# Optimization experiments

Hardware: AMD Instinct MI355X
Metric: run time of the kernel (lower is better)

Reference implementation:

```python
import jax, jax.numpy as jnp
import numpy as np

NODE_NUM = 6
C_IN = 1024
B = 16384
N_OPS = 9
TAU = 10.0
EPS = 1e-5
ACTS = (jax.nn.relu, jax.nn.sigmoid, jnp.tanh)


def setup_inputs() -> dict:
    key = jax.random.key(0)
    k = jax.random.split(key, 12)
    n_edges = NODE_NUM * (NODE_NUM + 1) // 2  # 21
    nB = n_edges - NODE_NUM  # 15 edges with cin=cout=C_IN//2

    def w(kk, shape, fan_in):
        return jax.random.normal(kk, shape, jnp.float32) / np.float32(np.sqrt(fan_in))

    return {
        "x": jax.random.normal(k[0], (B, C_IN), jnp.float32),
        "arch_params": 0.001 * jax.random.normal(k[1], (n_edges, N_OPS), jnp.float32),
        "gumbel": jax.random.gumbel(k[2], (n_edges, N_OPS), jnp.float32),
        "dense_w_A": w(k[3], (NODE_NUM, 3, C_IN // 2, C_IN), C_IN),
        "dense_b_A": 0.01 * jax.random.normal(k[4], (NODE_NUM, 3, C_IN // 2), jnp.float32),
        "group_w_A": w(k[5], (NODE_NUM, 3, 4, C_IN // 8, C_IN // 4), C_IN // 4),
        "group_b_A": 0.01 * jax.random.normal(k[6], (NODE_NUM, 3, C_IN // 2), jnp.float32),
        "pool_w_A": w(k[7], (NODE_NUM, 2, C_IN // 2, C_IN), C_IN),
        "dense_w_B": w(k[8], (nB, 3, C_IN // 2, C_IN // 2), C_IN // 2),
        "dense_b_B": 0.01 * jax.random.normal(k[9], (nB, 3, C_IN // 2), jnp.float32),
        "group_w_B": w(k[10], (nB, 3, 4, C_IN // 8, C_IN // 8), C_IN // 8),
        "group_b_B": 0.01 * jax.random.normal(k[11], (nB, 3, C_IN // 2), jnp.float32),
    }


def _batchnorm(h):
    # training-mode BatchNorm2d on [B, C, 1, 1] == normalize over batch, affine-free
    m = jnp.mean(h, axis=0, keepdims=True)
    v = jnp.var(h, axis=0, keepdims=True)
    return (h - m) * jax.lax.rsqrt(v + EPS)


def _apply_edge(h, op_idx, wscale, dw, db, gw, gb, pw):
    # h: [B, cin]; dw: [3, cout, cin]; gw: [3, 4, cout//4, cin//4]; pw: [2, cout, cin] or None
    cout = dw.shape[1]

    def pool(p):
        def f(hh):
            # ReLU-Conv1x1-BN preprocess when cin != cout, else identity
            y = _batchnorm(jax.nn.relu(hh) @ pw[p].T) if pw is not None else hh
            if p == 0:  # avg_pool_3x3 on 1x1 spatial, pad=1, count_include_pad
                y = y / 9.0
            # p == 1: max_pool_3x3 on 1x1 spatial is identity
            return _batchnorm(y)  # MixedOp-appended BatchNorm2d(affine=False)
        return f

    def dense(a):
        return lambda hh: ACTS[a](hh @ dw[a].T + db[a])

    def gdense(a):
        def f(hh):
            hg = hh.reshape(hh.shape[0], 4, -1)  # [B, 4, cin//4]
            y = jnp.einsum('bgi,goi->bgo', hg, gw[a]).reshape(hh.shape[0], -1) + gb[a]
            return ACTS[a](y)
        return f

    zero = lambda hh: jnp.zeros((hh.shape[0], cout), hh.dtype)
    branches = [pool(0), pool(1), dense(0), dense(1), dense(2),
                gdense(0), gdense(1), gdense(2), zero]
    return jax.lax.switch(op_idx, branches, h) * wscale


def reference(x, arch_params, gumbel, dense_w_A, dense_b_A, group_w_A, group_b_A,
              pool_w_A, dense_w_B, dense_b_B, group_w_B, group_b_B):
    # GDAS gumbel-softmax hard routing (straight-through)
    logits = (jax.nn.log_softmax(arch_params, axis=1) + gumbel) / TAU
    prob = jax.nn.softmax(logits, axis=1)
    index = jnp.argmax(prob, axis=1)                      # [n_edges]
    one_h = jax.nn.one_hot(index, N_OPS, dtype=prob.dtype)
    hardwts = one_h - jax.lax.stop_gradient(prob) + prob  # [n_edges, N_OPS]

    # arch rows are indexed by sorted edge-key order, matching torch edge2index
    keys = sorted('{}->{}'.format(j, i + 1) for i in range(NODE_NUM) for j in range(i + 1))
    e2i = {kk: n for n, kk in enumerate(keys)}

    states = [x]
    a_ct = 0
    b_ct = 0
    for i in range(1, NODE_NUM + 1):
        acc = None
        for j in range(i):
            e = e2i['{}->{}'.format(j, i)]
            w_e = hardwts[e, index[e]]
            if j == 0:
                out = _apply_edge(states[0], index[e], w_e, dense_w_A[a_ct], dense_b_A[a_ct],
                                  group_w_A[a_ct], group_b_A[a_ct], pool_w_A[a_ct])
                a_ct += 1
            else:
                out = _apply_edge(states[j], index[e], w_e, dense_w_B[b_ct], dense_b_B[b_ct],
                                  group_w_B[b_ct], group_b_B[b_ct], None)
                b_ct += 1
            acc = out if acc is None else acc + out
        states.append(acc)
    return states[-1]  # [B, C_IN//2]; final_linear is never applied in forward()
```

## Files before the change

### kernel.cpp

```cpp
#include <hip/hip_runtime.h>

#define BATCH 16384
#define CH 512
#define EPSBN 1e-5f

typedef __attribute__((ext_vector_type(8))) short short8;
typedef __attribute__((ext_vector_type(4))) float f32x4;
typedef __attribute__((ext_vector_type(4))) unsigned short ushort4v;

#define GLOAD16(gp, lp) __builtin_amdgcn_global_load_lds( \
    (const __attribute__((address_space(1))) void*)(gp),  \
    (__attribute__((address_space(3))) void*)(lp), 16, 0, 0)

__constant__ int d_etab[6][6] = {
  {0,0,0,0,0,0},
  {1,6,0,0,0,0},
  {2,7,11,0,0,0},
  {3,8,12,15,0,0},
  {4,9,13,16,18,0},
  {5,10,14,17,19,20}};
__constant__ int d_bct[21] = {0,0,0,0,0,0, 0,1,3,6,10, 2,4,7,11, 5,8,12, 9,13, 14};

static __device__ __forceinline__ long woff(int e){
  return (e < 6) ? (long)e*524288 : 3145728L + (long)d_bct[e]*262144;
}

static __device__ __forceinline__ unsigned short f2b(float f){
  union { float f; unsigned u; } v; v.f = f;
  unsigned r = v.u + 0x7fffu + ((v.u >> 16) & 1u);
  return (unsigned short)(r >> 16);
}
static __device__ __forceinline__ float b2f(unsigned short u){
  union { unsigned u; float f; } v; v.u = ((unsigned)u) << 16; return v.f;
}
static __device__ __forceinline__ float actf(int act, float v){
  if (act == 0) return fmaxf(v, 0.f);
  if (act == 1) return 1.f/(1.f + __expf(-v));
  float e = __expf(2.f*v);
  return 1.f - 2.f/(e + 1.f);
}

__global__ void k_sentinel(float* out){ out[0] = 1.0e6f; }

__global__ void k_index(const float* __restrict__ ap, const float* __restrict__ gum,
                        int* __restrict__ idx, float* __restrict__ wsc){
  int e = threadIdx.x;
  if (e >= 21) return;
  const float* a = ap + e*9;
  const float* g = gum + e*9;
  float m = a[0];
  for (int o=1;o<9;o++) m = fmaxf(m, a[o]);
  float s = 0.f;
  for (int o=0;o<9;o++) s += expf(a[o]-m);
  float lse = m + logf(s);
  float lg[9]; float lm = -1e30f;
  for (int o=0;o<9;o++){ lg[o] = (a[o]-lse+g[o]) / 10.0f; lm = fmaxf(lm, lg[o]); }
  float ss = 0.f;
  for (int o=0;o<9;o++) ss += expf(lg[o]-lm);
  int bi = 0; float bp = -1.f;
  for (int o=0;o<9;o++){
    float p = expf(lg[o]-lm)/ss;
    if (p > bp){ bp = p; bi = o; }
  }
  idx[e] = bi;
  wsc[e] = (1.0f - bp) + bp;
}

__global__ void k_f2b4(const float* __restrict__ in, unsigned short* __restrict__ outp, long n4){
  long stride = (long)gridDim.x*blockDim.x;
  for (long i = (long)blockIdx.x*blockDim.x + threadIdx.x; i < n4; i += stride){
    const float4 v = ((const float4*)in)[i];
    ushort4v o;
    o[0] = f2b(v.x); o[1] = f2b(v.y); o[2] = f2b(v.z); o[3] = f2b(v.w);
    ((ushort4v*)outp)[i] = o;
  }
}

__global__ void k_wconv_all(const int* __restrict__ idxp,
                            const float* __restrict__ dwA, const float* __restrict__ pwA,
                            const float* __restrict__ gwA, const float* __restrict__ dwB,
                            const float* __restrict__ gwB,
                            unsigned short* __restrict__ Wball){
  int e = blockIdx.x >> 7;
  int blk = blockIdx.x & 127;
  int id = idxp[e];
  const float* src; long n;
  if (e < 6){
    int a = e;
    if (id >= 2 && id <= 4){ n = 524288; src = dwA + ((long)a*3 + (id-2))*n; }
    else if (id < 2)       { n = 524288; src = pwA + ((long)a*2 + id)*n; }
    else if (id <= 7)      { n = 131072; src = gwA + ((long)a*3 + (id-5))*131072; }
    else return;
  } else {
    int b = d_bct[e];
    if (id >= 2 && id <= 4)     { n = 262144; src = dwB + ((long)b*3 + (id-2))*n; }
    else if (id >= 5 && id <= 7){ n = 65536;  src = gwB + ((long)b*3 + (id-5))*65536; }
    else return;
  }
  unsigned short* dst = Wball + woff(e);
  long n4 = n >> 2;
  long stride = 128*256;
  for (long i = (long)blk*256 + threadIdx.x; i < n4; i += stride){
    const float4 v = ((const float4*)src)[i];
    ushort4v o;
    o[0] = f2b(v.x); o[1] = f2b(v.y); o[2] = f2b(v.z); o[3] = f2b(v.w);
    ((ushort4v*)dst)[i] = o;
  }
}

__global__ __launch_bounds__(512, 4) void k_gemmA_all(
    const unsigned short* __restrict__ xb, const unsigned short* __restrict__ Wball,
    unsigned short* __restrict__ s0, unsigned short* __restrict__ s1,
    unsigned short* __restrict__ s2, unsigned short* __restrict__ s3,
    unsigned short* __restrict__ s4, unsigned short* __restrict__ pre6,
    const float* __restrict__ dbA, const float* __restrict__ gbA,
    const int* __restrict__ idxp, const float* __restrict__ wscp)
{
  int e = blockIdx.x >> 9;
  int id = idxp[e];
  if (id == 8) return;
  unsigned short* target;
  switch(e){ case 0: target=s0; break; case 1: target=s1; break; case 2: target=s2; break;
             case 3: target=s3; break; case 4: target=s4; break; default: target=pre6; }
  bool pool = (id < 2);
  bool grp = (id >= 5);
  int K = grp ? 256 : 1024;
  int act = pool ? 0 : (grp ? id-5 : id-2);
  float we = wscp[e];

  int inner = blockIdx.x & 511;
  int lg = (inner & 7) * 64 + (inner >> 3);
  int rowTile = lg >> 2, colTile = lg & 3;
  int row0 = rowTile * 128, col0 = colTile * 128;

  int t = threadIdx.x;
  int lane = t & 63, wave = t >> 6;
  int wm = wave >> 2, wn = wave & 3;
  int l16 = lane & 15, lq = lane >> 4;

  __shared__ unsigned short LDS[24576];

  int ra = t >> 2;
  int ca = (((t & 3) ^ ((ra >> 1) & 3)) << 3);
  int aoff[4], boff[2];
  #pragma unroll
  for (int m=0;m<4;m++){ int R = wm*64 + m*16 + l16; aoff[m] = R*32 + ((lq ^ ((R>>1)&3))<<3); }
  #pragma unroll
  for (int n=0;n<2;n++){ int C = wn*32 + n*16 + l16; boff[n] = C*32 + ((lq ^ ((C>>1)&3))<<3); }

  const unsigned short* Abase = xb + (grp ? (long)colTile*K : 0);
  const unsigned short* Wbase = Wball + (long)e*524288 + (long)col0*K;
  const unsigned short* gA = Abase + (long)(row0 + ra)*1024 + ca;
  const unsigned short* gB = Wbase + (long)ra*K + ca;
  const float* bias = (grp ? gbA : dbA) + ((long)e*3 + act)*CH;

  f32x4 acc[4][2];
  #pragma unroll
  for (int m=0;m<4;m++){ acc[m][0]=(f32x4){0,0,0,0}; acc[m][1]=(f32x4){0,0,0,0}; }

  auto STAGE = [&](int tile, int bsel){
    long kk = (long)tile*32;
    GLOAD16(gA + kk, &LDS[bsel*4096 + t*8]);
    GLOAD16(gB + kk, &LDS[12288 + bsel*4096 + t*8]);
  };

  int nk = K >> 5;
  STAGE(0, 0);
  STAGE(1, 1);
  int cb = 0;
  for (int kt = 0; kt < nk; ++kt){
    if (kt+1 < nk) { asm volatile("s_waitcnt vmcnt(2)" ::: "memory"); }
    else           { asm volatile("s_waitcnt vmcnt(0)" ::: "memory"); }
    __builtin_amdgcn_s_barrier();
    if (kt+2 < nk) STAGE(kt+2, (cb >= 1) ? cb-1 : cb+2);
    const unsigned short* pA = &LDS[cb*4096];
    const unsigned short* pB = &LDS[12288 + cb*4096];
    short8 a[4], b[2];
    #pragma unroll
    for (int m=0;m<4;m++){
      a[m] = *(const short8*)(pA + aoff[m]);
      if (pool){
        #pragma unroll
        for (int q=0;q<8;q++) a[m][q] = (a[m][q] < (short)0) ? (short)0 : a[m][q];
      }
    }
    #pragma unroll
    for (int n=0;n<2;n++) b[n] = *(const short8*)(pB + boff[n]);
    #pragma unroll
    for (int m=0;m<4;m++)
      #pragma unroll
      for (int n=0;n<2;n++)
        acc[m][n] = __builtin_amdgcn_mfma_f32_16x16x32_bf16(a[m], b[n], acc[m][n], 0,0,0);
    cb = (cb+1 == 3) ? 0 : cb+1;
  }

  #pragma unroll
  for (int n=0;n<2;n++){
    int cn = col0 + wn*32 + n*16 + l16;
    float bv = pool ? 0.f : bias[cn];
    #pragma unroll
    for (int m=0;m<4;m++)
      #pragma unroll
      for (int r=0;r<4;r++){
        int row = row0 + wm*64 + m*16 + lq*4 + r;
        long off = (long)row*CH + cn;
        if (pool) target[off] = f2b(acc[m][n][r]);
        else      target[off] = f2b(we * actf(act, acc[m][n][r] + bv));
      }
  }
}

__global__ __launch_bounds__(512) void k_statsA(
    const unsigned short* __restrict__ s0, const unsigned short* __restrict__ s1,
    const unsigned short* __restrict__ s2, const unsigned short* __restrict__ s3,
    const unsigned short* __restrict__ s4, const unsigned short* __restrict__ pre6,
    float* __restrict__ part, const int* __restrict__ idxp)
{
  int e = blockIdx.x >> 7;
  if (idxp[e] >= 2) return;
  const unsigned short* S;
  switch(e){ case 0: S=s0; break; case 1: S=s1; break; case 2: S=s2; break;
             case 3: S=s3; break; case 4: S=s4; break; default: S=pre6; }
  int blk = blockIdx.x & 127;
  int c = threadIdx.x;
  const unsigned short* p = S + (long)blk*128*CH + c;
  float s = 0.f, q = 0.f;
  for (int r = 0; r < 128; r++){ float v = b2f(p[(long)r*CH]); s += v; q += v*v; }
  long o = (((long)e*128 + blk)*CH + c)*2;
  part[o] = s; part[o+1] = q;
}

__global__ __launch_bounds__(512) void k_stats2A(
    const float* __restrict__ part, float* __restrict__ alphaAll,
    float* __restrict__ mvalAll, const int* __restrict__ idxp)
{
  int c = threadIdx.x;
  for (int e = 0; e < 6; ++e){
    int id = idxp[e];
    if (id >= 2) continue;
    float s = 0.f, q = 0.f;
    for (int b = 0; b < 128; b++){
      long o = (((long)e*128 + b)*CH + c)*2;
      s += part[o]; q += part[o+1];
    }
    float m = s * (1.f/16384.f);
    float v = q * (1.f/16384.f) - m*m;
    v = fmaxf(v, 0.f);
    float s1 = rsqrtf(v + EPSBN);
    float vz = v / (v + EPSBN);
    float al = (id==0) ? (s1 * (1.f/9.f) * rsqrtf(vz*(1.f/81.f) + EPSBN))
                       : (s1 * rsqrtf(vz + EPSBN));
    alphaAll[(long)e*CH + c] = al;
    mvalAll[(long)e*CH + c] = m;
  }
}

__global__ __launch_bounds__(512) void k_statsB_node(
    int node,
    const unsigned short* __restrict__ sb0, const unsigned short* __restrict__ sb1,
    const unsigned short* __restrict__ sb2, const unsigned short* __restrict__ sb3,
    const unsigned short* __restrict__ sb4,
    float* __restrict__ part, const int* __restrict__ idxp)
{
  int c = threadIdx.x;
  for (int jj = 1; jj < node; ++jj){
    int e = d_etab[node-1][jj];
    if (idxp[e] >= 2) continue;
    const unsigned short* S;
    switch(jj){ case 1: S=sb0; break; case 2: S=sb1; break;
                case 3: S=sb2; break; case 4: S=sb3; break; default: S=sb4; }
    const unsigned short* p = S + (long)blockIdx.x*128*CH + c;
    float s = 0.f, q = 0.f;
    for (int r = 0; r < 128; r++){ float v = b2f(p[(long)r*CH]); s += v; q += v*v; }
    long o = (((long)jj*128 + blockIdx.x)*CH + c)*2;
    part[o] = s; part[o+1] = q;
  }
}

__global__ __launch_bounds__(512) void k_stats2B_node(
    int node, const float* __restrict__ part,
    float* __restrict__ alphaAll, float* __restrict__ mvalAll,
    const int* __restrict__ idxp)
{
  int c = threadIdx.x;
  for (int jj = 1; jj < node; ++jj){
    int e = d_etab[node-1][jj];
    int id = idxp[e];
    if (id >= 2) continue;
    float s = 0.f, q = 0.f;
    for (int b = 0; b < 128; b++){
      long o = (((long)jj*128 + b)*CH + c)*2;
      s += part[o]; q += part[o+1];
    }
    float m = s * (1.f/16384.f);
    float v = q * (1.f/16384.f) - m*m;
    v = fmaxf(v, 0.f);
    float al = (id==0) ? ((1.f/9.f) * rsqrtf(v*(1.f/81.f) + EPSBN))
                       : rsqrtf(v + EPSBN);
    alphaAll[(long)e*CH + c] = al;
    mvalAll[(long)e*CH + c] = m;
  }
}

__global__ __launch_bounds__(512, 4) void k_fused(
    int node,
    const unsigned short* __restrict__ pre,
    const unsigned short* __restrict__ sb0, const unsigned short* __restrict__ sb1,
    const unsigned short* __restrict__ sb2, const unsigned short* __restrict__ sb3,
    const unsigned short* __restrict__ sb4,
    unsigned short* __restrict__ sbout, float* __restrict__ outf,
    const unsigned short* __restrict__ Wball,
    const float* __restrict__ dbB, const float* __restrict__ gbB,
    const float* __restrict__ alphaAll, const float* __restrict__ mvalAll,
    const int* __restrict__ idxp, const float* __restrict__ wscp)
{
  int bid = blockIdx.x;
  int lg = (bid & 7) * 64 + (bid >> 3);
  int rowTile = lg >> 2, colTile = lg & 3;
  int row0 = rowTile * 128, col0 = colTile * 128;

  int t = threadIdx.x;
  int lane = t & 63, wave = t >> 6;
  int wm = wave >> 2, wn = wave & 3;
  int l16 = lane & 15, lq = lane >> 4;

  __shared__ unsigned short LDS[24576];

  int ra = t >> 2;
  int ca = (((t & 3) ^ ((ra >> 1) & 3)) << 3);
  int aoff[4], boff[2];
  #pragma unroll
  for (int m=0;m<4;m++){ int R = wm*64 + m*16 + l16; aoff[m] = R*32 + ((lq ^ ((R>>1)&3))<<3); }
  #pragma unroll
  for (int n=0;n<2;n++){ int C = wn*32 + n*16 + l16; boff[n] = C*32 + ((lq ^ ((C>>1)&3))<<3); }

  f32x4 facc[4][2];
  #pragma unroll
  for (int m=0;m<4;m++){ facc[m][0]=(f32x4){0,0,0,0}; facc[m][1]=(f32x4){0,0,0,0}; }

  for (int jj = 0; jj < node; ++jj){
    int e = d_etab[node-1][jj];
    int id = idxp[e];
    if (id == 8) continue;
    float we = wscp[e];

    if (jj == 0){
      if (id < 2){
        const float* al = alphaAll + (long)e*CH;
        const float* mv = mvalAll + (long)e*CH;
        #pragma unroll
        for (int n=0;n<2;n++){
          int cn = col0 + wn*32 + n*16 + l16;
          float a_n = al[cn], m_n = mv[cn];
          #pragma unroll
          for (int m=0;m<4;m++){
            int rowb = row0 + wm*64 + m*16 + lq*4;
            #pragma unroll
            for (int r=0;r<4;r++)
              facc[m][n][r] += we * (b2f(pre[(long)(rowb+r)*CH + cn]) - m_n) * a_n;
          }
        }
      } else {
        #pragma unroll
        for (int n=0;n<2;n++){
          int cn = col0 + wn*32 + n*16 + l16;
          #pragma unroll
          for (int m=0;m<4;m++){
            int rowb = row0 + wm*64 + m*16 + lq*4;
            #pragma unroll
            for (int r=0;r<4;r++)
              facc[m][n][r] += b2f(pre[(long)(rowb+r)*CH + cn]);
          }
        }
      }
      continue;
    }

    const unsigned short* st;
    switch(jj){ case 1: st=sb0; break; case 2: st=sb1; break;
                case 3: st=sb2; break; case 4: st=sb3; break; default: st=sb4; }

    if (id < 2){
      const float* al = alphaAll + (long)e*CH;
      const float* mv = mvalAll + (long)e*CH;
      #pragma unroll
      for (int n=0;n<2;n++){
        int cn = col0 + wn*32 + n*16 + l16;
        float a_n = al[cn], m_n = mv[cn];
        #pragma unroll
        for (int m=0;m<4;m++){
          int rowb = row0 + wm*64 + m*16 + lq*4;
          #pragma unroll
          for (int r=0;r<4;r++)
            facc[m][n][r] += we * (b2f(st[(long)(rowb+r)*CH + cn]) - m_n) * a_n;
        }
      }
      continue;
    }

    bool grp = (id >= 5);
    int K = grp ? 128 : 512;
    int act = grp ? id - 5 : id - 2;
    const unsigned short* Abase = st + (grp ? (long)colTile*K : 0);
    const unsigned short* Wbase = Wball + woff(e) + (long)col0*K;
    const float* bias = (grp ? gbB : dbB) + ((long)d_bct[e]*3 + act)*CH;

    const unsigned short* gA = Abase + (long)(row0 + ra)*512 + ca;
    const unsigned short* gB = Wbase + (long)ra*K + ca;

    f32x4 acc[4][2];
    #pragma unroll
    for (int m=0;m<4;m++){ acc[m][0]=(f32x4){0,0,0,0}; acc[m][1]=(f32x4){0,0,0,0}; }

    auto STAGE = [&](int tile, int bsel){
      long kk = (long)tile*32;
      GLOAD16(gA + kk, &LDS[bsel*4096 + t*8]);
      GLOAD16(gB + kk, &LDS[12288 + bsel*4096 + t*8]);
    };

    int nk = K >> 5;
    __builtin_amdgcn_s_barrier();
    STAGE(0, 0);
    STAGE(1, 1);
    int cb = 0;
    for (int kt = 0; kt < nk; ++kt){
      if (kt+1 < nk) { asm volatile("s_waitcnt vmcnt(2)" ::: "memory"); }
      else           { asm volatile("s_waitcnt vmcnt(0)" ::: "memory"); }
      __builtin_amdgcn_s_barrier();
      if (kt+2 < nk) STAGE(kt+2, (cb >= 1) ? cb-1 : cb+2);
      const unsigned short* pA = &LDS[cb*4096];
      const unsigned short* pB = &LDS[12288 + cb*4096];
      short8 a[4], b[2];
      #pragma unroll
      for (int m=0;m<4;m++) a[m] = *(const short8*)(pA + aoff[m]);
      #pragma unroll
      for (int n=0;n<2;n++) b[n] = *(const short8*)(pB + boff[n]);
      #pragma unroll
      for (int m=0;m<4;m++)
        #pragma unroll
        for (int n=0;n<2;n++)
          acc[m][n] = __builtin_amdgcn_mfma_f32_16x16x32_bf16(a[m], b[n], acc[m][n], 0,0,0);
      cb = (cb+1 == 3) ? 0 : cb+1;
    }

    #pragma unroll
    for (int n=0;n<2;n++){
      int cn = col0 + wn*32 + n*16 + l16;
      float bv = bias[cn];
      #pragma unroll
      for (int m=0;m<4;m++)
        #pragma unroll
        for (int r=0;r<4;r++)
          facc[m][n][r] += we * actf(act, acc[m][n][r] + bv);
    }
  }

  #pragma unroll
  for (int n=0;n<2;n++){
    int cn = col0 + wn*32 + n*16 + l16;
    #pragma unroll
    for (int m=0;m<4;m++){
      int rowb = row0 + wm*64 + m*16 + lq*4;
      #pragma unroll
      for (int r=0;r<4;r++){
        long off = (long)(rowb+r)*CH + cn;
        if (node == 6) outf[off] = facc[m][n][r];
        else           sbout[off] = f2b(facc[m][n][r]);
      }
    }
  }
}

extern "C" void kernel_launch(void* const* d_in, const int* in_sizes, int n_in,
                              void* d_out, int out_size, void* d_ws, size_t ws_size,
                              hipStream_t stream)
{
  const float* x   = (const float*)d_in[0];
  const float* ap  = (const float*)d_in[1];
  const float* gum = (const float*)d_in[2];
  const float* dwA = (const float*)d_in[3];
  const float* dbA = (const float*)d_in[4];
  const float* gwA = (const float*)d_in[5];
  const float* gbA = (const float*)d_in[6];
  const float* pwA = (const float*)d_in[7];
  const float* dwB = (const float*)d_in[8];
  const float* dbB = (const float*)d_in[9];
  const float* gwB = (const float*)d_in[10];
  const float* gbB = (const float*)d_in[11];
  float* out = (float*)d_out;

  char* ws = (char*)d_ws;
  size_t cur = 0;
  auto alloc = [&](size_t bytes)->void*{
    size_t o = cur; cur += (bytes + 255) & ~(size_t)255; return (void*)(ws + o);
  };
  int*   idx      = (int*)  alloc(21*sizeof(int));
  float* wsc      = (float*)alloc(21*sizeof(float));
  float* alphaAll = (float*)alloc((size_t)21*CH*sizeof(float));
  float* mvalAll  = (float*)alloc((size_t)21*CH*sizeof(float));
  float* part     = (float*)alloc((size_t)6*128*CH*2*sizeof(float));
  unsigned short* Wball = (unsigned short*)alloc((size_t)7077888*sizeof(unsigned short));
  unsigned short* pre6  = (unsigned short*)alloc((size_t)BATCH*CH*sizeof(unsigned short));
  unsigned short* xb    = (unsigned short*)alloc((size_t)BATCH*1024*sizeof(unsigned short));
  unsigned short* sb[5];
  for (int i=0;i<5;i++)
    sb[i] = (unsigned short*)alloc((size_t)BATCH*CH*sizeof(unsigned short));

  if (cur > ws_size){
    hipLaunchKernelGGL(k_sentinel, dim3(1), dim3(1), 0, stream, out);
    return;
  }

  hipLaunchKernelGGL(k_f2b4, dim3(2048), dim3(256), 0, stream, x, xb, (long)BATCH*1024/4);
  hipLaunchKernelGGL(k_index, dim3(1), dim3(32), 0, stream, ap, gum, idx, wsc);
  hipLaunchKernelGGL(k_wconv_all, dim3(21*128), dim3(256), 0, stream,
                     idx, dwA, pwA, gwA, dwB, gwB, Wball);

  hipLaunchKernelGGL(k_gemmA_all, dim3(6*512), dim3(512), 0, stream,
                     xb, Wball, sb[0], sb[1], sb[2], sb[3], sb[4], pre6,
                     dbA, gbA, idx, wsc);
  hipLaunchKernelGGL(k_statsA, dim3(6*128), dim3(512), 0, stream,
                     sb[0], sb[1], sb[2], sb[3], sb[4], pre6, part, idx);
  hipLaunchKernelGGL(k_stats2A, dim3(1), dim3(512), 0, stream,
                     part, alphaAll, mvalAll, idx);

  hipLaunchKernelGGL(k_fused, dim3(512), dim3(512), 0, stream,
                     1, sb[0], sb[0], sb[1], sb[2], sb[3], sb[4],
                     sb[0], out, Wball, dbB, gbB, alphaAll, mvalAll, idx, wsc);
  for (int node = 2; node <= 6; node++){
    hipLaunchKernelGGL(k_statsB_node, dim3(128), dim3(512), 0, stream,
                       node, sb[0], sb[1], sb[2], sb[3], sb[4], part, idx);
    hipLaunchKernelGGL(k_stats2B_node, dim3(1), dim3(512), 0, stream,
                       node, part, alphaAll, mvalAll, idx);
    const unsigned short* pre = (node < 6) ? sb[node-1] : pre6;
    unsigned short* sbout = (node < 6) ? sb[node-1] : sb[0] ;
    hipLaunchKernelGGL(k_fused, dim3(512), dim3(512), 0, stream,
                       node, pre, sb[0], sb[1], sb[2], sb[3], sb[4],
                       sbout, out, Wball, dbB, gbB, alphaAll, mvalAll, idx, wsc);
  }
}
```

Measured before the change: 455.2 us.

## Fuse batchnorm column statistics into GEMM epilogues via atomics and drop stats kernels

Column sum and sum-of-squares for batchnorm are now accumulated in the GEMM and fused-node epilogues with wave shuffles and float atomics into a small zeroed buffer. This removes the separate stats and stats2 kernels, which re-read each bf16 state tensor. A new k_fix1 kernel replaces the node-1 fused launch: it normalises state 1 in place and computes its stats. Consumers derive mean and alpha directly from the accumulated sums. The trade-off is atomic contention and non-deterministic summation order, plus stats computed from fp32 values before bf16 rounding.

```diff
diff --git a/kernel.cpp b/kernel.cpp
--- a/kernel.cpp
+++ b/kernel.cpp
@@ -38,6 +38,34 @@
   if (act == 1) return 1.f/(1.f + __expf(-v));
   float e = __expf(2.f*v);
   return 1.f - 2.f/(e + 1.f);
+}
+
+static __device__ __forceinline__ void col_stats_atomic(
+    float vs, float vq, int cn, int slot, float* partw){
+  vs += __shfl_xor(vs, 16); vs += __shfl_xor(vs, 32);
+  vq += __shfl_xor(vq, 16); vq += __shfl_xor(vq, 32);
+  if (((threadIdx.x) & 63) < 16){
+    atomicAdd(&partw[((long)slot*CH + cn)*2    ], vs);
+    atomicAdd(&partw[((long)slot*CH + cn)*2 + 1], vq);
+  }
+}
+
+static __device__ __forceinline__ void ms_from(const float* part, int slot, int cn,
+                                               float& mu, float& var){
+  long sl = ((long)slot*CH + cn)*2;
+  float s = part[sl], q = part[sl+1];
+  mu = s * (1.f/16384.f);
+  var = fmaxf(q * (1.f/16384.f) - mu*mu, 0.f);
+}
+static __device__ __forceinline__ float alphaA(int id, float v){
+  float s1r = rsqrtf(v + EPSBN);
+  float vz = v / (v + EPSBN);
+  return (id==0) ? (s1r * (1.f/9.f) * rsqrtf(vz*(1.f/81.f) + EPSBN))
+                 : (s1r * rsqrtf(vz + EPSBN));
+}
+static __device__ __forceinline__ float alphaB(int id, float v){
+  return (id==0) ? ((1.f/9.f) * rsqrtf(v*(1.f/81.f) + EPSBN))
+                 : rsqrtf(v + EPSBN);
 }
 
 __global__ void k_sentinel(float* out){ out[0] = 1.0e6f; }
@@ -114,7 +142,8 @@
     unsigned short* __restrict__ s2, unsigned short* __restrict__ s3,
     unsigned short* __restrict__ s4, unsigned short* __restrict__ pre6,
     const float* __restrict__ dbA, const float* __restrict__ gbA,
-    const int* __restrict__ idxp, const float* __restrict__ wscp)
+    const int* __restrict__ idxp, const float* __restrict__ wscp,
+    float* __restrict__ partw)
 {
   int e = blockIdx.x >> 9;
   int id = idxp[e];
@@ -198,107 +227,61 @@
   for (int n=0;n<2;n++){
     int cn = col0 + wn*32 + n*16 + l16;
     float bv = pool ? 0.f : bias[cn];
+    float cs = 0.f, cq = 0.f;
     #pragma unroll
     for (int m=0;m<4;m++)
       #pragma unroll
       for (int r=0;r<4;r++){
         int row = row0 + wm*64 + m*16 + lq*4 + r;
         long off = (long)row*CH + cn;
-        if (pool) target[off] = f2b(acc[m][n][r]);
-        else      target[off] = f2b(we * actf(act, acc[m][n][r] + bv));
+        float v = pool ? acc[m][n][r] : (we * actf(act, acc[m][n][r] + bv));
+        target[off] = f2b(v);
+        cs += v; cq += v*v;
       }
-  }
-}
-
-__global__ __launch_bounds__(512) void k_statsA(
-    const unsigned short* __restrict__ s0, const unsigned short* __restrict__ s1,
-    const unsigned short* __restrict__ s2, const unsigned short* __restrict__ s3,
-    const unsigned short* __restrict__ s4, const unsigned short* __restrict__ pre6,
-    float* __restrict__ part, const int* __restrict__ idxp)
+    col_stats_atomic(cs, cq, cn, e, partw);
+  }
+}
+
+__global__ __launch_bounds__(512, 4) void k_fix1(
+    unsigned short* __restrict__ s1, const float* __restrict__ part,
+    float* __restrict__ partw, const int* __restrict__ idxp,
+    const float* __restrict__ wscp)
 {
-  int e = blockIdx.x >> 7;
-  if (idxp[e] >= 2) return;
-  const unsigned short* S;
-  switch(e){ case 0: S=s0; break; case 1: S=s1; break; case 2: S=s2; break;
-             case 3: S=s3; break; case 4: S=s4; break; default: S=pre6; }
-  int blk = blockIdx.x & 127;
-  int c = threadIdx.x;
-  const unsigned short* p = S + (long)blk*128*CH + c;
-  float s = 0.f, q = 0.f;
-  for (int r = 0; r < 128; r++){ float v = b2f(p[(long)r*CH]); s += v; q += v*v; }
-  long o = (((long)e*128 + blk)*CH + c)*2;
-  part[o] = s; part[o+1] = q;
-}
-
-__global__ __launch_bounds__(512) void k_stats2A(
-    const float* __restrict__ part, float* __restrict__ alphaAll,
-    float* __restrict__ mvalAll, const int* __restrict__ idxp)
-{
-  int c = threadIdx.x;
-  for (int e = 0; e < 6; ++e){
-    int id = idxp[e];
-    if (id >= 2) continue;
-    float s = 0.f, q = 0.f;
-    for (int b = 0; b < 128; b++){
-      long o = (((long)e*128 + b)*CH + c)*2;
-      s += part[o]; q += part[o+1];
-    }
-    float m = s * (1.f/16384.f);
-    float v = q * (1.f/16384.f) - m*m;
-    v = fmaxf(v, 0.f);
-    float s1 = rsqrtf(v + EPSBN);
-    float vz = v / (v + EPSBN);
-    float al = (id==0) ? (s1 * (1.f/9.f) * rsqrtf(vz*(1.f/81.f) + EPSBN))
-                       : (s1 * rsqrtf(vz + EPSBN));
-    alphaAll[(long)e*CH + c] = al;
-    mvalAll[(long)e*CH + c] = m;
-  }
-}
-
-__global__ __launch_bounds__(512) void k_statsB_node(
-    int node,
-    const unsigned short* __restrict__ sb0, const unsigned short* __restrict__ sb1,
-    const unsigned short* __restrict__ sb2, const unsigned short* __restrict__ sb3,
-    const unsigned short* __restrict__ sb4,
-    float* __restrict__ part, const int* __restrict__ idxp)
-{
-  int c = threadIdx.x;
-  for (int jj = 1; jj < node; ++jj){
-    int e = d_etab[node-1][jj];
-    if (idxp[e] >= 2) continue;
-    const unsigned short* S;
-    switch(jj){ case 1: S=sb0; break; case 2: S=sb1; break;
-                case 3: S=sb2; break; case 4: S=sb3; break; default: S=sb4; }
-    const unsigned short* p = S + (long)blockIdx.x*128*CH + c;
-    float s = 0.f, q = 0.f;
-    for (int r = 0; r < 128; r++){ float v = b2f(p[(long)r*CH]); s += v; q += v*v; }
-    long o = (((long)jj*128 + blockIdx.x)*CH + c)*2;
-    part[o] = s; part[o+1] = q;
-  }
-}
-
-__global__ __launch_bounds__(512) void k_stats2B_node(
-    int node, const float* __restrict__ part,
-    float* __restrict__ alphaAll, float* __restrict__ mvalAll,
-    const int* __restrict__ idxp)
-{
-  int c = threadIdx.x;
-  for (int jj = 1; jj < node; ++jj){
-    int e = d_etab[node-1][jj];
-    int id = idxp[e];
-    if (id >= 2) continue;
-    float s = 0.f, q = 0.f;
-    for (int b = 0; b < 128; b++){
-      long o = (((long)jj*128 + b)*CH + c)*2;
-      s += part[o]; q += part[o+1];
-    }
-    float m = s * (1.f/16384.f);
-    float v = q * (1.f/16384.f) - m*m;
-    v = fmaxf(v, 0.f);
-    float al = (id==0) ? ((1.f/9.f) * rsqrtf(v*(1.f/81.f) + EPSBN))
-                       : rsqrtf(v + EPSBN);
-    alphaAll[(long)e*CH + c] = al;
-    mvalAll[(long)e*CH + c] = m;
+  int id = idxp[0];
+  float we = wscp[0];
+
+  int bid = blockIdx.x;
+  int lg = (bid & 7) * 64 + (bid >> 3);
+  int rowTile = lg >> 2, colTile = lg & 3;
+  int row0 = rowTile * 128, col0 = colTile * 128;
+
+  int t = threadIdx.x;
+  int lane = t & 63, wave = t >> 6;
+  int wm = wave >> 2, wn = wave & 3;
+  int l16 = lane & 15, lq = lane >> 4;
+
+  #pragma unroll
+  for (int n=0;n<2;n++){
+    int cn = col0 + wn*32 + n*16 + l16;
+    float cs = 0.f, cq = 0.f;
+    float mu = 0.f, al = 0.f;
+    if (id < 2){
+      float var; ms_from(part, 0, cn, mu, var);
+      al = alphaA(id, var);
+    }
+    #pragma unroll
+    for (int m=0;m<4;m++)
+      #pragma unroll
+      for (int r=0;r<4;r++){
+        int row = row0 + wm*64 + m*16 + lq*4 + r;
+        long off = (long)row*CH + cn;
+        float v;
+        if (id == 8){ v = 0.f; s1[off] = 0; }
+        else if (id < 2){ v = we * (b2f(s1[off]) - mu) * al; s1[off] = f2b(v); }
+        else { v = b2f(s1[off]); }
+        cs += v; cq += v*v;
+      }
+    col_stats_atomic(cs, cq, cn, 6+1, partw);
   }
 }
 
@@ -311,7 +294,7 @@
     unsigned short* __restrict__ sbout, float* __restrict__ outf,
     const unsigned short* __restrict__ Wball,
     const float* __restrict__ dbB, const float* __restrict__ gbB,
-    const float* __restrict__ alphaAll, const float* __restrict__ mvalAll,
+    const float* __restrict__ part, float* __restrict__ partw,
     const int* __restrict__ idxp, const float* __restrict__ wscp)
 {
   int bid = blockIdx.x;
@@ -346,18 +329,17 @@
 
     if (jj == 0){
       if (id < 2){
-        const float* al = alphaAll + (long)e*CH;
-        const float* mv = mvalAll + (long)e*CH;
         #pragma unroll
         for (int n=0;n<2;n++){
           int cn = col0 + wn*32 + n*16 + l16;
-          float a_n = al[cn], m_n = mv[cn];
+          float mu, var; ms_from(part, e, cn, mu, var);
+          float al = alphaA(id, var);
           #pragma unroll
           for (int m=0;m<4;m++){
             int rowb = row0 + wm*64 + m*16 + lq*4;
             #pragma unroll
             for (int r=0;r<4;r++)
-              facc[m][n][r] += we * (b2f(pre[(long)(rowb+r)*CH + cn]) - m_n) * a_n;
+              facc[m][n][r] += we * (b2f(pre[(long)(rowb+r)*CH + cn]) - mu) * al;
           }
         }
       } else {
@@ -381,18 +363,17 @@
                 case 3: st=sb2; break; case 4: st=sb3; break; default: st=sb4; }
 
     if (id < 2){
-      const float* al = alphaAll + (long)e*CH;
-      const float* mv = mvalAll + (long)e*CH;
       #pragma unroll
       for (int n=0;n<2;n++){
         int cn = col0 + wn*32 + n*16 + l16;
-        float a_n = al[cn], m_n = mv[cn];
+        float mu, var; ms_from(part, 6+jj, cn, mu, var);
+        float al = alphaB(id, var);
         #pragma unroll
         for (int m=0;m<4;m++){
           int rowb = row0 + wm*64 + m*16 + lq*4;
           #pragma unroll
           for (int r=0;r<4;r++)
-            facc[m][n][r] += we * (b2f(st[(long)(rowb+r)*CH + cn]) - m_n) * a_n;
+            facc[m][n][r] += we * (b2f(st[(long)(rowb+r)*CH + cn]) - mu) * al;
         }
       }
       continue;
@@ -458,16 +439,19 @@
   #pragma unroll
   for (int n=0;n<2;n++){
     int cn = col0 + wn*32 + n*16 + l16;
+    float cs = 0.f, cq = 0.f;
     #pragma unroll
     for (int m=0;m<4;m++){
       int rowb = row0 + wm*64 + m*16 + lq*4;
       #pragma unroll
       for (int r=0;r<4;r++){
         long off = (long)(rowb+r)*CH + cn;
-        if (node == 6) outf[off] = facc[m][n][r];
-        else           sbout[off] = f2b(facc[m][n][r]);
+        float v = facc[m][n][r];
+        if (node == 6) outf[off] = v;
+        else { sbout[off] = f2b(v); cs += v; cq += v*v; }
       }
     }
+    if (node < 6) col_stats_atomic(cs, cq, cn, 6+node, partw);
   }
 }
 
@@ -494,11 +478,9 @@
   auto alloc = [&](size_t bytes)->void*{
     size_t o = cur; cur += (bytes + 255) & ~(size_t)255; return (void*)(ws + o);
   };
-  int*   idx      = (int*)  alloc(21*sizeof(int));
-  float* wsc      = (float*)alloc(21*sizeof(float));
-  float* alphaAll = (float*)alloc((size_t)21*CH*sizeof(float));
-  float* mvalAll  = (float*)alloc((size_t)21*CH*sizeof(float));
-  float* part     = (float*)alloc((size_t)6*128*CH*2*sizeof(float));
+  int*   idx  = (int*)  alloc(21*sizeof(int));
+  float* wsc  = (float*)alloc(21*sizeof(float));
+  float* part = (float*)alloc((size_t)12*CH*2*sizeof(float));
   unsigned short* Wball = (unsigned short*)alloc((size_t)7077888*sizeof(unsigned short));
   unsigned short* pre6  = (unsigned short*)alloc((size_t)BATCH*CH*sizeof(unsigned short));
   unsigned short* xb    = (unsigned short*)alloc((size_t)BATCH*1024*sizeof(unsigned short));
@@ -511,6 +493,7 @@
     return;
   }
 
+  hipMemsetAsync(part, 0, (size_t)12*CH*2*sizeof(float), stream);
   hipLaunchKernelGGL(k_f2b4, dim3(2048), dim3(256), 0, stream, x, xb, (long)BATCH*1024/4);
   hipLaunchKernelGGL(k_index, dim3(1), dim3(32), 0, stream, ap, gum, idx, wsc);
   hipLaunchKernelGGL(k_wconv_all, dim3(21*128), dim3(256), 0, stream,
@@ -518,24 +501,15 @@
 
   hipLaunchKernelGGL(k_gemmA_all, dim3(6*512), dim3(512), 0, stream,
                      xb, Wball, sb[0], sb[1], sb[2], sb[3], sb[4], pre6,
-                     dbA, gbA, idx, wsc);
-  hipLaunchKernelGGL(k_statsA, dim3(6*128), dim3(512), 0, stream,
-                     sb[0], sb[1], sb[2], sb[3], sb[4], pre6, part, idx);
-  hipLaunchKernelGGL(k_stats2A, dim3(1), dim3(512), 0, stream,
-                     part, alphaAll, mvalAll, idx);
-
-  hipLaunchKernelGGL(k_fused, dim3(512), dim3(512), 0, stream,
-                     1, sb[0], sb[0], sb[1], sb[2], sb[3], sb[4],
-                     sb[0], out, Wball, dbB, gbB, alphaAll, mvalAll, idx, wsc);
+                     dbA, gbA, idx, wsc, part);
+  hipLaunchKernelGGL(k_fix1, dim3(512), dim3(512), 0, stream,
+                     sb[0], part, part, idx, wsc);
+
   for (int node = 2; node <= 6; node++){
-    hipLaunchKernelGGL(k_statsB_node, dim3(128), dim3(512), 0, stream,
-                       node, sb[0], sb[1], sb[2], sb[3], sb[4], part, idx);
-    hipLaunchKernelGGL(k_stats2B_node, dim3(1), dim3(512), 0, stream,
-                       node, part, alphaAll, mvalAll, idx);
     const unsigned short* pre = (node < 6) ? sb[node-1] : pre6;
     unsigned short* sbout = (node < 6) ? sb[node-1] : sb[0] ;
     hipLaunchKernelGGL(k_fused, dim3(512), dim3(512), 0, stream,
                        node, pre, sb[0], sb[1], sb[2], sb[3], sb[4],
-                       sbout, out, Wball, dbB, gbB, alphaAll, mvalAll, idx, wsc);
-  }
-}
+                       sbout, out, Wball, dbB, gbB, part, part, idx, wsc);
+  }
+}
```

Result: faster. 426.5 us (-6.3%).
